# Performance work log

Hardware: AMD Instinct MI355X
Metric: run time of the kernel (lower is better)

## Reference

```python
import jax, jax.numpy as jnp
import numpy as np

B, S, D = 2, 2048, 1024
H = 16
HD = D // H  # 64


def setup_inputs() -> dict:
    key = jax.random.key(0)
    k1, k2, k3, k4, k5, k6 = jax.random.split(key, 6)
    hidden_states = jax.random.normal(k1, (B, S, D), dtype=jnp.float32)
    attention_mask = jax.random.randint(k2, (B, S), 0, 2, dtype=jnp.int32)
    scale = 1.0 / np.sqrt(D)
    Wq = jax.random.normal(k3, (D, D), dtype=jnp.float32) * scale
    bq = jax.random.normal(k4, (D,), dtype=jnp.float32) * 0.02
    Wk = jax.random.normal(k5, (D, D), dtype=jnp.float32) * scale
    bk = jax.random.normal(k6, (D,), dtype=jnp.float32) * 0.02
    return {"hidden_states": hidden_states, "attention_mask": attention_mask,
            "Wq": Wq, "bq": bq, "Wk": Wk, "bk": bk}


def _split_heads(x):
    # [B, S, D] -> [B, H, S, HD]
    b, s, _ = x.shape
    return x.reshape(b, s, H, HD).transpose(0, 2, 1, 3)


def reference(hidden_states, attention_mask, Wq, bq, Wk, bk):
    dh = jnp.sqrt(jnp.float32(HD))
    q = _split_heads(hidden_states @ Wq + bq)            # [B,H,S,HD]
    k = _split_heads(hidden_states @ Wk + bk)            # [B,H,S,HD]
    v = q + k                                            # value = Q + K
    k_t = -jax.nn.log_sigmoid(-k)                        # negate the logsigmoid(-K) transform
    scores = jnp.einsum('bhqd,bhkd->bhqk', q, k_t) / dh  # [B,H,S,S]
    # mask applied on the QUERY axis (dim 2), broadcast over key axis (faithful to source)
    mask = (attention_mask[:, None, :, None] == 0)       # [B,1,S,1]
    scores = jnp.where(mask, jnp.float32(-10000.0), scores)
    probs = jax.nn.softmax(scores, axis=-1)              # dropout: eval mode (identity)
    ctx = jnp.einsum('bhqk,bhkd->bhqd', probs, v)        # [B,H,S,HD]
    ctx = ctx.transpose(0, 2, 1, 3).reshape(B, S, D)
    return ctx
```

## Files before the change

kernel.cpp:

```cpp
#include <hip/hip_runtime.h>
#include <hip/hip_bf16.h>

#define B_ 2
#define S_ 2048
#define D_ 1024
#define H_ 16
#define HD_ 64

typedef __attribute__((ext_vector_type(8))) short short8;
typedef __attribute__((ext_vector_type(4))) short short4v;
typedef __attribute__((ext_vector_type(4))) float float4v;

typedef const __attribute__((address_space(1))) void* gas_ptr;
typedef __attribute__((address_space(3))) void* las_ptr;

static __device__ inline void gl_lds16(const void* g, void* l) {
  __builtin_amdgcn_global_load_lds((gas_ptr)g, (las_ptr)l, 16, 0, 0);
}

static __device__ inline float b2f(__hip_bfloat16 h) { return __bfloat162float(h); }

static __device__ inline short f2bs(float x) {
  __hip_bfloat16 h = __float2bfloat16(x);
  union { __hip_bfloat16 h; short s; } u; u.h = h; return u.s;
}
static __device__ inline float bs2f(short s) {
  union { short s; __hip_bfloat16 h; } u; u.s = s; return __bfloat162float(u.h);
}
static __device__ inline short4v pk4(float a, float b, float c, float d) {
  union { __hip_bfloat162 h[2]; short4v s; } u;
  u.h[0] = __float22bfloat162_rn(float2{a, b});
  u.h[1] = __float22bfloat162_rn(float2{c, d});
  return u.s;
}

static __device__ inline float4v mfma32(short8 a, short8 b, float4v c) {
  return __builtin_amdgcn_mfma_f32_16x16x32_bf16(a, b, c, 0, 0, 0);
}
static __device__ inline float4v mfma16(short4v a, short4v b, float4v c) {
  return __builtin_amdgcn_mfma_f32_16x16x16bf16_1k(a, b, c, 0, 0, 0);
}

__global__ __launch_bounds__(256) void pre(
    const float* __restrict__ Wq, const float* __restrict__ Wk,
    const float* __restrict__ hs,
    __hip_bfloat16* __restrict__ Wqt, __hip_bfloat16* __restrict__ Wkt,
    __hip_bfloat16* __restrict__ hsb) {
  if (blockIdx.z == 2) {
    const int blk = blockIdx.y * 16 + blockIdx.x;
    for (int it = 0; it < 8; ++it) {
      const size_t i = (size_t)blk * 16384 + it * 2048 + threadIdx.x * 8;
      const float4v v0 = *(const float4v*)(hs + i);
      const float4v v1 = *(const float4v*)(hs + i + 4);
      short8 s;
      for (int j = 0; j < 4; ++j) { s[j] = f2bs(v0[j]); s[4 + j] = f2bs(v1[j]); }
      *(short8*)(hsb + i) = s;
    }
    return;
  }
  const float* W = blockIdx.z ? Wk : Wq;
  __hip_bfloat16* Wt = blockIdx.z ? Wkt : Wqt;
  __shared__ float t[64][65];
  const int n0 = blockIdx.x * 64, k0 = blockIdx.y * 64;
  const int c = threadIdx.x & 63, r0 = threadIdx.x >> 6;
  for (int i = 0; i < 16; ++i) {
    const int r = i * 4 + r0;
    t[c][r] = W[(size_t)(k0 + r) * D_ + n0 + c];
  }
  __syncthreads();
  for (int i = 0; i < 16; ++i) {
    const int rr = i * 4 + r0;
    Wt[(size_t)(n0 + rr) * D_ + k0 + c] = __float2bfloat16(t[rr][c]);
  }
}

__global__ __launch_bounds__(256) void gemm_fused(
    const __hip_bfloat16* __restrict__ A,
    const __hip_bfloat16* __restrict__ Wqt, const __hip_bfloat16* __restrict__ Wkt,
    const float* __restrict__ bq, const float* __restrict__ bk,
    __hip_bfloat16* __restrict__ q_out, __hip_bfloat16* __restrict__ kt_out,
    __hip_bfloat16* __restrict__ vT) {
  const int n0 = blockIdx.x * 128, m0 = blockIdx.y * 64;
  __shared__ __hip_bfloat16 As[2][64 * 32];
  __shared__ __hip_bfloat16 Bq[2][128 * 32];
  __shared__ __hip_bfloat16 Bk[2][128 * 32];
  const int tid = threadIdx.x, wid = tid >> 6, lane = tid & 63;
  const int wm = (wid >> 1) * 32, wn = (wid & 1) * 64;
  const int l15 = lane & 15, l4 = lane >> 4;
  const float4v zz = {0.f, 0.f, 0.f, 0.f};
  float4v accq[2][4], acck[2][4];
  for (int i = 0; i < 2; ++i)
    for (int j = 0; j < 4; ++j) { accq[i][j] = zz; acck[i][j] = zz; }
  const int arow = wid * 16 + (lane >> 2);
  const int brow = wid * 32 + (lane >> 2);
  const int lk8 = (lane & 3) * 8;
  gl_lds16(A + (size_t)(m0 + arow) * D_ + lk8, As[0] + wid * 512);
  gl_lds16(Wqt + (size_t)(n0 + brow) * D_ + lk8, Bq[0] + wid * 1024);
  gl_lds16(Wqt + (size_t)(n0 + brow + 16) * D_ + lk8, Bq[0] + wid * 1024 + 512);
  gl_lds16(Wkt + (size_t)(n0 + brow) * D_ + lk8, Bk[0] + wid * 1024);
  gl_lds16(Wkt + (size_t)(n0 + brow + 16) * D_ + lk8, Bk[0] + wid * 1024 + 512);
  int p = 0;
  for (int kb = 0; kb < 32; ++kb) {
    __syncthreads();
    if (kb < 31) {
      const int kc = (kb + 1) * 32 + lk8;
      gl_lds16(A + (size_t)(m0 + arow) * D_ + kc, As[p ^ 1] + wid * 512);
      gl_lds16(Wqt + (size_t)(n0 + brow) * D_ + kc, Bq[p ^ 1] + wid * 1024);
      gl_lds16(Wqt + (size_t)(n0 + brow + 16) * D_ + kc, Bq[p ^ 1] + wid * 1024 + 512);
      gl_lds16(Wkt + (size_t)(n0 + brow) * D_ + kc, Bk[p ^ 1] + wid * 1024);
      gl_lds16(Wkt + (size_t)(n0 + brow + 16) * D_ + kc, Bk[p ^ 1] + wid * 1024 + 512);
    }
    short8 af[2], bfq[4], bfk[4];
    const int fo = l4 * 8;
    for (int rt = 0; rt < 2; ++rt)
      af[rt] = *(const short8*)(As[p] + (wm + rt * 16 + l15) * 32 + fo);
    for (int ct = 0; ct < 4; ++ct) {
      bfq[ct] = *(const short8*)(Bq[p] + (wn + ct * 16 + l15) * 32 + fo);
      bfk[ct] = *(const short8*)(Bk[p] + (wn + ct * 16 + l15) * 32 + fo);
    }
    for (int rt = 0; rt < 2; ++rt)
      for (int ct = 0; ct < 4; ++ct) {
        accq[rt][ct] = mfma32(af[rt], bfq[ct], accq[rt][ct]);
        acck[rt][ct] = mfma32(af[rt], bfk[ct], acck[rt][ct]);
      }
    p ^= 1;
  }
  float bvq[4], bvk[4];
  for (int ct = 0; ct < 4; ++ct) {
    bvq[ct] = bq[n0 + wn + ct * 16 + l15];
    bvk[ct] = bk[n0 + wn + ct * 16 + l15];
  }
  for (int rt = 0; rt < 2; ++rt)
    for (int ct = 0; ct < 4; ++ct) {
      const int col = n0 + wn + ct * 16 + l15;
      const int h = col >> 6, d = col & 63;
      const int rowb = m0 + wm + rt * 16 + l4 * 4;
      short4v vv;
      for (int r = 0; r < 4; ++r) {
        const int row = rowb + r;
        const float qv = accq[rt][ct][r] + bvq[ct];
        const float kv = acck[rt][ct][r] + bvk[ct];
        const float sp = fmaxf(kv, 0.f) + __logf(1.f + __expf(-fabsf(kv)));
        q_out[(size_t)row * D_ + col] = __float2bfloat16(qv);
        kt_out[(size_t)row * D_ + col] = __float2bfloat16(sp);
        vv[r] = f2bs(qv + kv);
      }
      const int b = rowb >> 11, s = rowb & 2047;
      const int sw = (s & ~63) | (((s >> 4) & 3) << 2) | (((s >> 2) & 3) << 4);
      *(short4v*)(vT + ((size_t)(b * H_ + h) * HD_ + d) * S_ + sw) = vv;
    }
}

__global__ __launch_bounds__(256, 4) void attn(
    const __hip_bfloat16* __restrict__ qb, const __hip_bfloat16* __restrict__ ktb,
    const __hip_bfloat16* __restrict__ vT, const int* __restrict__ mask,
    float* __restrict__ out) {
  __shared__ short smem[17664];
  const int id = blockIdx.x;
  const int xcd = id & 7;
  const int rest = id >> 3;
  const int q0 = (rest & 15) * 128;
  const int hb = (rest >> 4) * 8 + xcd;
  const int h = hb >> 1, b = hb & 1;
  const int tid = threadIdx.x, wid = tid >> 6, lane = tid & 63;
  const int l15 = lane & 15, l4 = lane >> 4;
  const __hip_bfloat16* qh = qb + (size_t)b * S_ * D_ + h * HD_;
  const __hip_bfloat16* kh = ktb + (size_t)b * S_ * D_ + h * HD_;
  const __hip_bfloat16* vh = vT + (size_t)(b * H_ + h) * HD_ * S_;
  const int srow = tid >> 2;
  const int b0 = tid & 3;
  const int sh = srow & 7;
  const int w0 = srow * 64 + ((b0 ^ sh) * 8);
  const int w1 = srow * 64 + (((b0 + 4) ^ sh) * 8);

  const int qlA = wid * 32 + l15, qlB = qlA + 16;
  const int qrA = q0 + qlA, qrB = q0 + qlB;
  const float SC = 0.125f * 1.44269504f;
  const float mqA = (mask[b * S_ + qrA] != 0) ? SC : 0.f;
  const float mqB = (mask[b * S_ + qrB] != 0) ? SC : 0.f;
  const short8 rA0 = *(const short8*)(qh + (size_t)qrA * D_ + l4 * 8);
  const short8 rA1 = *(const short8*)(qh + (size_t)qrA * D_ + 32 + l4 * 8);
  const short8 rB0 = *(const short8*)(qh + (size_t)qrB * D_ + l4 * 8);
  const short8 rB1 = *(const short8*)(qh + (size_t)qrB * D_ + 32 + l4 * 8);
  short8 bqA0, bqA1, bqB0, bqB1;
  for (int j = 0; j < 8; ++j) {
    bqA0[j] = f2bs(bs2f(rA0[j]) * mqA);
    bqA1[j] = f2bs(bs2f(rA1[j]) * mqA);
    bqB0[j] = f2bs(bs2f(rB0[j]) * mqB);
    bqB1[j] = f2bs(bs2f(rB1[j]) * mqB);
  }

  const int lsh = l15 & 7;
  const int ak0off = l15 * 64 + ((l4 ^ lsh) * 8);
  const int ak1off = l15 * 64 + (((l4 + 4) ^ lsh) * 8);
  const int vb0off = 4096 + ((2 * l4) ^ lsh) * 8;
  const int vb1off = 4096 + ((2 * l4 + 1) ^ lsh) * 8;

  const float4v zz = {0.f, 0.f, 0.f, 0.f};
  float4v oaccA[4] = {zz, zz, zz, zz};
  float4v oaccB[4] = {zz, zz, zz, zz};
  float lsumA = 0.f, lsumB = 0.f;

  short8 gk0 = *(const short8*)(kh + (size_t)srow * D_ + b0 * 8);
  short8 gk1 = *(const short8*)(kh + (size_t)srow * D_ + b0 * 8 + 32);
  short8 gv0 = *(const short8*)(vh + (size_t)srow * S_ + b0 * 8);
  short8 gv1 = *(const short8*)(vh + (size_t)srow * S_ + b0 * 8 + 32);

  int p = 0;
  for (int c = 0; c < 32; ++c) {
    short* bufp = smem + p * 8192;
    *(short8*)(bufp + w0) = gk0;
    *(short8*)(bufp + w1) = gk1;
    *(short8*)(bufp + 4096 + w0) = gv0;
    *(short8*)(bufp + 4096 + w1) = gv1;
    __syncthreads();
    if (c < 31) {
      const int kb = (c + 1) * 64;
      gk0 = *(const short8*)(kh + (size_t)(kb + srow) * D_ + b0 * 8);
      gk1 = *(const short8*)(kh + (size_t)(kb + srow) * D_ + b0 * 8 + 32);
      gv0 = *(const short8*)(vh + (size_t)srow * S_ + kb + b0 * 8);
      gv1 = *(const short8*)(vh + (size_t)srow * S_ + kb + b0 * 8 + 32);
    }
    short4v pA[4], pB[4];
#pragma unroll
    for (int t = 0; t < 4; ++t) {
      const short8 ak0 = *(const short8*)(bufp + t * 1024 + ak0off);
      const short8 ak1 = *(const short8*)(bufp + t * 1024 + ak1off);
      float4v cA = zz, cB = zz;
      cA = mfma32(ak0, bqA0, cA);
      cA = mfma32(ak1, bqA1, cA);
      cB = mfma32(ak0, bqB0, cB);
      cB = mfma32(ak1, bqB1, cB);
      float eA[4], eB[4];
#pragma unroll
      for (int r = 0; r < 4; ++r) {
        eA[r] = __builtin_amdgcn_exp2f(cA[r]); lsumA += eA[r];
        eB[r] = __builtin_amdgcn_exp2f(cB[r]); lsumB += eB[r];
      }
      pA[t] = pk4(eA[0], eA[1], eA[2], eA[3]);
      pB[t] = pk4(eB[0], eB[1], eB[2], eB[3]);
    }
#pragma unroll
    for (int dt = 0; dt < 4; ++dt) {
      const int rb = (dt * 16 + l15) * 64;
      const short8 av0 = *(const short8*)(bufp + rb + vb0off);
      const short8 av1 = *(const short8*)(bufp + rb + vb1off);
      const short4v a0 = {av0[0], av0[1], av0[2], av0[3]};
      const short4v a1 = {av0[4], av0[5], av0[6], av0[7]};
      const short4v a2 = {av1[0], av1[1], av1[2], av1[3]};
      const short4v a3 = {av1[4], av1[5], av1[6], av1[7]};
      oaccA[dt] = mfma16(a0, pA[0], oaccA[dt]);
      oaccB[dt] = mfma16(a0, pB[0], oaccB[dt]);
      oaccA[dt] = mfma16(a1, pA[1], oaccA[dt]);
      oaccB[dt] = mfma16(a1, pB[1], oaccB[dt]);
      oaccA[dt] = mfma16(a2, pA[2], oaccA[dt]);
      oaccB[dt] = mfma16(a2, pB[2], oaccB[dt]);
      oaccA[dt] = mfma16(a3, pA[3], oaccA[dt]);
      oaccB[dt] = mfma16(a3, pB[3], oaccB[dt]);
    }
    p ^= 1;
  }
  float lA = lsumA + __shfl_xor(lsumA, 16); lA += __shfl_xor(lA, 32);
  float lB = lsumB + __shfl_xor(lsumB, 16); lB += __shfl_xor(lB, 32);
  __syncthreads();
  float* mbuf = (float*)smem;
  float* mlb = (float*)smem + 128 * 68;
#pragma unroll
  for (int dt = 0; dt < 4; ++dt)
#pragma unroll
    for (int r = 0; r < 4; ++r) {
      mbuf[qlA * 68 + dt * 16 + l4 * 4 + r] = oaccA[dt][r];
      mbuf[qlB * 68 + dt * 16 + l4 * 4 + r] = oaccB[dt][r];
    }
  if (l4 == 0) { mlb[qlA] = lA; mlb[qlB] = lB; }
  __syncthreads();
  const int qq = tid >> 1;
  const int dg = (tid & 1) * 32;
  const float li = 1.f / mlb[qq];
  float* orow = out + (size_t)(b * S_ + q0 + qq) * D_ + h * HD_ + dg;
#pragma unroll
  for (int i = 0; i < 8; ++i) {
    float4v v = *(const float4v*)&mbuf[qq * 68 + dg + i * 4];
#pragma unroll
    for (int r = 0; r < 4; ++r) v[r] *= li;
    *(float4v*)(orow + i * 4) = v;
  }
}

extern "C" void kernel_launch(void* const* d_in, const int* in_sizes, int n_in,
                              void* d_out, int out_size, void* d_ws, size_t ws_size,
                              hipStream_t stream) {
  const float* hs = (const float*)d_in[0];
  const int* mask = (const int*)d_in[1];
  const float* Wq = (const float*)d_in[2];
  const float* bq = (const float*)d_in[3];
  const float* Wk = (const float*)d_in[4];
  const float* bk = (const float*)d_in[5];
  float* out = (float*)d_out;
  char* ws = (char*)d_ws;
  const size_t MB = 1u << 20;
  __hip_bfloat16* q_b = (__hip_bfloat16*)(ws + 0 * MB);
  __hip_bfloat16* k_b = (__hip_bfloat16*)(ws + 8 * MB);
  __hip_bfloat16* hsb = (__hip_bfloat16*)(ws + 16 * MB);
  __hip_bfloat16* vT  = (__hip_bfloat16*)(ws + 24 * MB);
  __hip_bfloat16* Wqt = (__hip_bfloat16*)(ws + 32 * MB);
  __hip_bfloat16* Wkt = (__hip_bfloat16*)(ws + 34 * MB);

  pre<<<dim3(16, 16, 3), 256, 0, stream>>>(Wq, Wk, hs, Wqt, Wkt, hsb);
  gemm_fused<<<dim3(8, 64), 256, 0, stream>>>(hsb, Wqt, Wkt, bq, bk, q_b, k_b, vT);
  attn<<<dim3(512), 256, 0, stream>>>(q_b, k_b, vT, mask, out);
}
```

Baseline: 166.7 us.

## Enlarge QK projection GEMM tile and process two key blocks per attention barrier

The fused Q/K projection GEMM moves from a 64x128 tile with 256 threads to a 128x128 tile with 512 threads (8 waves), so each block loads weights once for twice as many rows and issues fewer loads per thread. The attention kernel now stages 128 keys and values per double-buffered iteration instead of 64, halving the number of loop iterations and __syncthreads barriers. In exchange, the attention kernel uses 64KB of LDS with occupancy hint lowered to 2 and holds twice as many prefetch registers, and the GEMM grid shrinks to 256 blocks, which may reduce latency hiding.

```diff
diff --git a/kernel.cpp b/kernel.cpp
--- a/kernel.cpp
+++ b/kernel.cpp
@@ -74,14 +74,14 @@
   }
 }
 
-__global__ __launch_bounds__(256) void gemm_fused(
+__global__ __launch_bounds__(512, 2) void gemm_fused(
     const __hip_bfloat16* __restrict__ A,
     const __hip_bfloat16* __restrict__ Wqt, const __hip_bfloat16* __restrict__ Wkt,
     const float* __restrict__ bq, const float* __restrict__ bk,
     __hip_bfloat16* __restrict__ q_out, __hip_bfloat16* __restrict__ kt_out,
     __hip_bfloat16* __restrict__ vT) {
-  const int n0 = blockIdx.x * 128, m0 = blockIdx.y * 64;
-  __shared__ __hip_bfloat16 As[2][64 * 32];
+  const int n0 = blockIdx.x * 128, m0 = blockIdx.y * 128;
+  __shared__ __hip_bfloat16 As[2][128 * 32];
   __shared__ __hip_bfloat16 Bq[2][128 * 32];
   __shared__ __hip_bfloat16 Bk[2][128 * 32];
   const int tid = threadIdx.x, wid = tid >> 6, lane = tid & 63;
@@ -91,24 +91,19 @@
   float4v accq[2][4], acck[2][4];
   for (int i = 0; i < 2; ++i)
     for (int j = 0; j < 4; ++j) { accq[i][j] = zz; acck[i][j] = zz; }
-  const int arow = wid * 16 + (lane >> 2);
-  const int brow = wid * 32 + (lane >> 2);
+  const int lrow = wid * 16 + (lane >> 2);
   const int lk8 = (lane & 3) * 8;
-  gl_lds16(A + (size_t)(m0 + arow) * D_ + lk8, As[0] + wid * 512);
-  gl_lds16(Wqt + (size_t)(n0 + brow) * D_ + lk8, Bq[0] + wid * 1024);
-  gl_lds16(Wqt + (size_t)(n0 + brow + 16) * D_ + lk8, Bq[0] + wid * 1024 + 512);
-  gl_lds16(Wkt + (size_t)(n0 + brow) * D_ + lk8, Bk[0] + wid * 1024);
-  gl_lds16(Wkt + (size_t)(n0 + brow + 16) * D_ + lk8, Bk[0] + wid * 1024 + 512);
+  gl_lds16(A + (size_t)(m0 + lrow) * D_ + lk8, As[0] + wid * 512);
+  gl_lds16(Wqt + (size_t)(n0 + lrow) * D_ + lk8, Bq[0] + wid * 512);
+  gl_lds16(Wkt + (size_t)(n0 + lrow) * D_ + lk8, Bk[0] + wid * 512);
   int p = 0;
   for (int kb = 0; kb < 32; ++kb) {
     __syncthreads();
     if (kb < 31) {
       const int kc = (kb + 1) * 32 + lk8;
-      gl_lds16(A + (size_t)(m0 + arow) * D_ + kc, As[p ^ 1] + wid * 512);
-      gl_lds16(Wqt + (size_t)(n0 + brow) * D_ + kc, Bq[p ^ 1] + wid * 1024);
-      gl_lds16(Wqt + (size_t)(n0 + brow + 16) * D_ + kc, Bq[p ^ 1] + wid * 1024 + 512);
-      gl_lds16(Wkt + (size_t)(n0 + brow) * D_ + kc, Bk[p ^ 1] + wid * 1024);
-      gl_lds16(Wkt + (size_t)(n0 + brow + 16) * D_ + kc, Bk[p ^ 1] + wid * 1024 + 512);
+      gl_lds16(A + (size_t)(m0 + lrow) * D_ + kc, As[p ^ 1] + wid * 512);
+      gl_lds16(Wqt + (size_t)(n0 + lrow) * D_ + kc, Bq[p ^ 1] + wid * 512);
+      gl_lds16(Wkt + (size_t)(n0 + lrow) * D_ + kc, Bk[p ^ 1] + wid * 512);
     }
     short8 af[2], bfq[4], bfk[4];
     const int fo = l4 * 8;
@@ -151,11 +146,11 @@
     }
 }
 
-__global__ __launch_bounds__(256, 4) void attn(
+__global__ __launch_bounds__(256, 2) void attn(
     const __hip_bfloat16* __restrict__ qb, const __hip_bfloat16* __restrict__ ktb,
     const __hip_bfloat16* __restrict__ vT, const int* __restrict__ mask,
     float* __restrict__ out) {
-  __shared__ short smem[17664];
+  __shared__ short smem[32768];
   const int id = blockIdx.x;
   const int xcd = id & 7;
   const int rest = id >> 3;
@@ -193,70 +188,85 @@
   const int lsh = l15 & 7;
   const int ak0off = l15 * 64 + ((l4 ^ lsh) * 8);
   const int ak1off = l15 * 64 + (((l4 + 4) ^ lsh) * 8);
-  const int vb0off = 4096 + ((2 * l4) ^ lsh) * 8;
-  const int vb1off = 4096 + ((2 * l4 + 1) ^ lsh) * 8;
+  const int vb0off = ((2 * l4) ^ lsh) * 8;
+  const int vb1off = ((2 * l4 + 1) ^ lsh) * 8;
 
   const float4v zz = {0.f, 0.f, 0.f, 0.f};
   float4v oaccA[4] = {zz, zz, zz, zz};
   float4v oaccB[4] = {zz, zz, zz, zz};
   float lsumA = 0.f, lsumB = 0.f;
 
-  short8 gk0 = *(const short8*)(kh + (size_t)srow * D_ + b0 * 8);
-  short8 gk1 = *(const short8*)(kh + (size_t)srow * D_ + b0 * 8 + 32);
-  short8 gv0 = *(const short8*)(vh + (size_t)srow * S_ + b0 * 8);
-  short8 gv1 = *(const short8*)(vh + (size_t)srow * S_ + b0 * 8 + 32);
+  short8 gk0[2], gk1[2], gv0[2], gv1[2];
+#pragma unroll
+  for (int u = 0; u < 2; ++u) {
+    gk0[u] = *(const short8*)(kh + (size_t)(u * 64 + srow) * D_ + b0 * 8);
+    gk1[u] = *(const short8*)(kh + (size_t)(u * 64 + srow) * D_ + b0 * 8 + 32);
+    gv0[u] = *(const short8*)(vh + (size_t)srow * S_ + u * 64 + b0 * 8);
+    gv1[u] = *(const short8*)(vh + (size_t)srow * S_ + u * 64 + b0 * 8 + 32);
+  }
 
   int p = 0;
-  for (int c = 0; c < 32; ++c) {
-    short* bufp = smem + p * 8192;
-    *(short8*)(bufp + w0) = gk0;
-    *(short8*)(bufp + w1) = gk1;
-    *(short8*)(bufp + 4096 + w0) = gv0;
-    *(short8*)(bufp + 4096 + w1) = gv1;
+  for (int c = 0; c < 16; ++c) {
+    short* bufp = smem + p * 16384;
+#pragma unroll
+    for (int u = 0; u < 2; ++u) {
+      *(short8*)(bufp + u * 4096 + w0) = gk0[u];
+      *(short8*)(bufp + u * 4096 + w1) = gk1[u];
+      *(short8*)(bufp + 8192 + u * 4096 + w0) = gv0[u];
+      *(short8*)(bufp + 8192 + u * 4096 + w1) = gv1[u];
+    }
     __syncthreads();
-    if (c < 31) {
-      const int kb = (c + 1) * 64;
-      gk0 = *(const short8*)(kh + (size_t)(kb + srow) * D_ + b0 * 8);
-      gk1 = *(const short8*)(kh + (size_t)(kb + srow) * D_ + b0 * 8 + 32);
-      gv0 = *(const short8*)(vh + (size_t)srow * S_ + kb + b0 * 8);
-      gv1 = *(const short8*)(vh + (size_t)srow * S_ + kb + b0 * 8 + 32);
-    }
-    short4v pA[4], pB[4];
-#pragma unroll
-    for (int t = 0; t < 4; ++t) {
-      const short8 ak0 = *(const short8*)(bufp + t * 1024 + ak0off);
-      const short8 ak1 = *(const short8*)(bufp + t * 1024 + ak1off);
-      float4v cA = zz, cB = zz;
-      cA = mfma32(ak0, bqA0, cA);
-      cA = mfma32(ak1, bqA1, cA);
-      cB = mfma32(ak0, bqB0, cB);
-      cB = mfma32(ak1, bqB1, cB);
-      float eA[4], eB[4];
-#pragma unroll
-      for (int r = 0; r < 4; ++r) {
-        eA[r] = __builtin_amdgcn_exp2f(cA[r]); lsumA += eA[r];
-        eB[r] = __builtin_amdgcn_exp2f(cB[r]); lsumB += eB[r];
-      }
-      pA[t] = pk4(eA[0], eA[1], eA[2], eA[3]);
-      pB[t] = pk4(eB[0], eB[1], eB[2], eB[3]);
-    }
-#pragma unroll
-    for (int dt = 0; dt < 4; ++dt) {
-      const int rb = (dt * 16 + l15) * 64;
-      const short8 av0 = *(const short8*)(bufp + rb + vb0off);
-      const short8 av1 = *(const short8*)(bufp + rb + vb1off);
-      const short4v a0 = {av0[0], av0[1], av0[2], av0[3]};
-      const short4v a1 = {av0[4], av0[5], av0[6], av0[7]};
-      const short4v a2 = {av1[0], av1[1], av1[2], av1[3]};
-      const short4v a3 = {av1[4], av1[5], av1[6], av1[7]};
-      oaccA[dt] = mfma16(a0, pA[0], oaccA[dt]);
-      oaccB[dt] = mfma16(a0, pB[0], oaccB[dt]);
-      oaccA[dt] = mfma16(a1, pA[1], oaccA[dt]);
-      oaccB[dt] = mfma16(a1, pB[1], oaccB[dt]);
-      oaccA[dt] = mfma16(a2, pA[2], oaccA[dt]);
-      oaccB[dt] = mfma16(a2, pB[2], oaccB[dt]);
-      oaccA[dt] = mfma16(a3, pA[3], oaccA[dt]);
-      oaccB[dt] = mfma16(a3, pB[3], oaccB[dt]);
+    if (c < 15) {
+      const int kb = (c + 1) * 128;
+#pragma unroll
+      for (int u = 0; u < 2; ++u) {
+        gk0[u] = *(const short8*)(kh + (size_t)(kb + u * 64 + srow) * D_ + b0 * 8);
+        gk1[u] = *(const short8*)(kh + (size_t)(kb + u * 64 + srow) * D_ + b0 * 8 + 32);
+        gv0[u] = *(const short8*)(vh + (size_t)srow * S_ + kb + u * 64 + b0 * 8);
+        gv1[u] = *(const short8*)(vh + (size_t)srow * S_ + kb + u * 64 + b0 * 8 + 32);
+      }
+    }
+#pragma unroll
+    for (int u = 0; u < 2; ++u) {
+      const short* kbase = bufp + u * 4096;
+      const short* vbase = bufp + 8192 + u * 4096;
+      short4v pA[4], pB[4];
+#pragma unroll
+      for (int t = 0; t < 4; ++t) {
+        const short8 ak0 = *(const short8*)(kbase + t * 1024 + ak0off);
+        const short8 ak1 = *(const short8*)(kbase + t * 1024 + ak1off);
+        float4v cA = zz, cB = zz;
+        cA = mfma32(ak0, bqA0, cA);
+        cA = mfma32(ak1, bqA1, cA);
+        cB = mfma32(ak0, bqB0, cB);
+        cB = mfma32(ak1, bqB1, cB);
+        float eA[4], eB[4];
+#pragma unroll
+        for (int r = 0; r < 4; ++r) {
+          eA[r] = __builtin_amdgcn_exp2f(cA[r]); lsumA += eA[r];
+          eB[r] = __builtin_amdgcn_exp2f(cB[r]); lsumB += eB[r];
+        }
+        pA[t] = pk4(eA[0], eA[1], eA[2], eA[3]);
+        pB[t] = pk4(eB[0], eB[1], eB[2], eB[3]);
+      }
+#pragma unroll
+      for (int dt = 0; dt < 4; ++dt) {
+        const int rb = (dt * 16 + l15) * 64;
+        const short8 av0 = *(const short8*)(vbase + rb + vb0off);
+        const short8 av1 = *(const short8*)(vbase + rb + vb1off);
+        const short4v a0 = {av0[0], av0[1], av0[2], av0[3]};
+        const short4v a1 = {av0[4], av0[5], av0[6], av0[7]};
+        const short4v a2 = {av1[0], av1[1], av1[2], av1[3]};
+        const short4v a3 = {av1[4], av1[5], av1[6], av1[7]};
+        oaccA[dt] = mfma16(a0, pA[0], oaccA[dt]);
+        oaccB[dt] = mfma16(a0, pB[0], oaccB[dt]);
+        oaccA[dt] = mfma16(a1, pA[1], oaccA[dt]);
+        oaccB[dt] = mfma16(a1, pB[1], oaccB[dt]);
+        oaccA[dt] = mfma16(a2, pA[2], oaccA[dt]);
+        oaccB[dt] = mfma16(a2, pB[2], oaccB[dt]);
+        oaccA[dt] = mfma16(a3, pA[3], oaccA[dt]);
+        oaccB[dt] = mfma16(a3, pB[3], oaccB[dt]);
+      }
     }
     p ^= 1;
   }
@@ -307,6 +317,6 @@
   __hip_bfloat16* Wkt = (__hip_bfloat16*)(ws + 34 * MB);
 
   pre<<<dim3(16, 16, 3), 256, 0, stream>>>(Wq, Wk, hs, Wqt, Wkt, hsb);
-  gemm_fused<<<dim3(8, 64), 256, 0, stream>>>(hsb, Wqt, Wkt, bq, bk, q_b, k_b, vT);
+  gemm_fused<<<dim3(8, 32), 512, 0, stream>>>(hsb, Wqt, Wkt, bq, bk, q_b, k_b, vT);
   attn<<<dim3(512), 256, 0, stream>>>(q_b, k_b, vT, mask, out);
 }
```

Result: no change. 164.9 us (-1.1%).
